# Performance work log

Measured on AMD Instinct MI355X. Metric: run time of the kernel, lower is better.

The kernel has to match this reference:

```python
import jax, jax.numpy as jnp
import numpy as np

D_MODEL = 1024
H = 16
D_K = D_MODEL // H  # 64


def setup_inputs() -> dict:
    key = jax.random.key(0)
    ks = jax.random.split(key, 10)
    s = 1.0 / np.sqrt(D_MODEL)
    x = jax.random.normal(ks[0], (4, 2048, D_MODEL), dtype=jnp.float32)
    # Per-head linear weights stacked: [H, d_model, d_k]
    Wq = jax.random.uniform(ks[1], (H, D_MODEL, D_K), jnp.float32, -s, s)
    bq = jax.random.uniform(ks[2], (H, D_K), jnp.float32, -s, s)
    Wk = jax.random.uniform(ks[3], (H, D_MODEL, D_K), jnp.float32, -s, s)
    bk = jax.random.uniform(ks[4], (H, D_K), jnp.float32, -s, s)
    Wv = jax.random.uniform(ks[5], (H, D_MODEL, D_K), jnp.float32, -s, s)
    bv = jax.random.uniform(ks[6], (H, D_K), jnp.float32, -s, s)
    so = 1.0 / np.sqrt(H * D_K)
    Wo = jax.random.uniform(ks[7], (H * D_K, D_MODEL), jnp.float32, -so, so)
    bo = jax.random.uniform(ks[8], (D_MODEL,), jnp.float32, -so, so)
    return {"x": x, "Wq": Wq, "bq": bq, "Wk": Wk, "bk": bk, "Wv": Wv, "bv": bv, "Wo": Wo, "bo": bo}


def reference(x, Wq, bq, Wk, bk, Wv, bv, Wo, bo):
    # x: [B, S, D]; Wq/Wk/Wv: [H, D, d_k]; b*: [H, d_k]
    q = jnp.einsum('bsd,hdk->bhsk', x, Wq) + bq[None, :, None, :]
    k = jnp.einsum('bsd,hdk->bhsk', x, Wk) + bk[None, :, None, :]
    v = jnp.einsum('bsd,hdk->bhsk', x, Wv) + bv[None, :, None, :]
    scores = jnp.einsum('bhqk,bhsk->bhqs', q, k) / np.sqrt(D_K)
    S = x.shape[1]
    causal = jnp.triu(jnp.ones((S, S), dtype=bool), k=1)  # True above diagonal
    scores = jnp.where(causal, -jnp.inf, scores)
    attn = jax.nn.softmax(scores, axis=-1)
    ctx = jnp.einsum('bhqs,bhsk->bhqk', attn, v)  # [B, H, S, d_k]
    B = x.shape[0]
    # concat heads: torch cats head outputs along last dim -> [B, S, H*d_k]
    ctx = jnp.transpose(ctx, (0, 2, 1, 3)).reshape(B, S, H * D_K)
    return ctx @ Wo + bo
```

## Files before the change

### kernel.cpp

```cpp
#include <hip/hip_runtime.h>
#include <hip/hip_bf16.h>

typedef unsigned short u16;
typedef __attribute__((ext_vector_type(8))) short short8;
typedef __attribute__((ext_vector_type(4))) short short4v;
typedef __attribute__((ext_vector_type(4))) float floatx4;

#define D_MODEL 1024
#define NH 16
#define SEQ 2048
#define BATCH 4
#define M_ROWS 8192
#define N_QKV 3072
#define PS_LD 72

#define QSCALE 0.18033688011112042f
#define EXP2_OFF 11.541560327111707f

__device__ __forceinline__ u16 f2u(float f) {
    __hip_bfloat16 h = __float2bfloat16(f);
    u16 u; __builtin_memcpy(&u, &h, 2); return u;
}

__device__ __forceinline__ void async_copy16(const u16* g, u16* l) {
    __builtin_amdgcn_global_load_lds(
        (const __attribute__((address_space(1))) unsigned int*)(g),
        (__attribute__((address_space(3))) unsigned int*)(l),
        16, 0, 0);
}

__global__ __launch_bounds__(256) void prep(
    const float* __restrict__ x,
    const float* __restrict__ Wq, const float* __restrict__ Wk,
    const float* __restrict__ Wv, const float* __restrict__ Wo,
    const float* __restrict__ bq, const float* __restrict__ bk,
    const float* __restrict__ bv, const float* __restrict__ bo,
    u16* __restrict__ xb, u16* __restrict__ Wpt, u16* __restrict__ Wot,
    float* __restrict__ biasp)
{
    __shared__ u16 T[64 * 72];
    const int tid = threadIdx.x;
    const int blk = blockIdx.x;

    if (blk < 4096) {
        size_t i = ((size_t)blk * 256 + tid) * 8;
        float4 f0 = *(const float4*)&x[i];
        float4 f1 = *(const float4*)&x[i + 4];
        u16 t[8] = {f2u(f0.x), f2u(f0.y), f2u(f0.z), f2u(f0.w),
                    f2u(f1.x), f2u(f1.y), f2u(f1.z), f2u(f1.w)};
        *(short8*)&xb[i] = *(short8*)t;
        return;
    }
    if (blk == 5120) {
        #pragma unroll
        for (int j = 0; j < 16; j++) {
            int idx = j * 256 + tid;
            float v;
            if (idx < 1024)      v = bq[idx] * QSCALE;
            else if (idx < 2048) v = bk[idx - 1024];
            else if (idx < 3072) v = bv[idx - 2048];
            else                 v = bo[idx - 3072];
            biasp[idx] = v;
        }
        return;
    }
    const int wb = blk - 4096;
    const int r = tid >> 2, s4 = (tid & 3) * 16;
    if (wb < 768) {
        int sel = wb / 256, rem = wb % 256;
        int h = rem >> 4, ktile = rem & 15;
        const float* W = (sel == 0) ? Wq : ((sel == 1) ? Wk : Wv);
        const float scale = (sel == 0) ? QSCALE : 1.0f;
        const float* src = W + ((size_t)h * 1024 + ktile * 64 + r) * 64 + s4;
        #pragma unroll
        for (int i = 0; i < 16; i++) T[(s4 + i) * 72 + r] = f2u(src[i] * scale);
        __syncthreads();
        u16 tmp[16];
        #pragma unroll
        for (int i = 0; i < 16; i++) tmp[i] = T[r * 72 + s4 + i];
        u16* dst = Wpt + ((size_t)sel * 1024 + h * 64 + r) * 1024 + ktile * 64 + s4;
        *(short8*)&dst[0] = *(short8*)&tmp[0];
        *(short8*)&dst[8] = *(short8*)&tmp[8];
    } else {
        int rem = wb - 768;
        int nt = rem >> 4, kt2 = rem & 15;
        const float* src = Wo + ((size_t)kt2 * 64 + r) * 1024 + nt * 64 + s4;
        #pragma unroll
        for (int i = 0; i < 16; i++) T[(s4 + i) * 72 + r] = f2u(src[i]);
        __syncthreads();
        u16 tmp[16];
        #pragma unroll
        for (int i = 0; i < 16; i++) tmp[i] = T[r * 72 + s4 + i];
        u16* dst = Wot + ((size_t)nt * 64 + r) * 1024 + kt2 * 64 + s4;
        *(short8*)&dst[0] = *(short8*)&tmp[0];
        *(short8*)&dst[8] = *(short8*)&tmp[8];
    }
}

__global__ __launch_bounds__(256) void vtrans(const u16* __restrict__ QKV,
                                              u16* __restrict__ Vtg) {
    __shared__ u16 T[64 * 72];
    const int bh = blockIdx.x, kt = blockIdx.y;
    const int b = bh >> 4, h = bh & 15;
    const int tid = threadIdx.x;
    const int r = tid >> 2, s4 = (tid & 3) * 16;
    const u16* vp = QKV + (size_t)(b * SEQ + kt * 64 + r) * N_QKV + 2 * D_MODEL + h * 64 + s4;
    *(short8*)&T[r * 72 + s4]     = *(const short8*)&vp[0];
    *(short8*)&T[r * 72 + s4 + 8] = *(const short8*)&vp[8];
    __syncthreads();
    u16 tmp[16];
    #pragma unroll
    for (int i = 0; i < 16; i++) tmp[i] = T[(s4 + i) * 72 + r];
    u16* op = Vtg + ((size_t)bh * 64 + r) * SEQ + kt * 64 + s4;
    *(short8*)&op[0] = *(short8*)&tmp[0];
    *(short8*)&op[8] = *(short8*)&tmp[8];
}

template <typename OT>
__global__ __launch_bounds__(256) void gemm128(
    const u16* __restrict__ A, const u16* __restrict__ Bt,
    const float* __restrict__ bias, OT* __restrict__ C,
    int M, int N, int K)
{
    __shared__ u16 As[128 * 64];
    __shared__ u16 Bs[128 * 64];
    const int tid = threadIdx.x;
    const int w = tid >> 6, lane = tid & 63;
    const int l16 = lane & 15, quad = lane >> 4;

    const int nwgx = gridDim.x;
    const int nwg = nwgx * gridDim.y;
    const int lin = blockIdx.y * nwgx + blockIdx.x;
    const int cpx = nwg >> 3;
    const int swz = (lin & 7) * cpx + (lin >> 3);
    const int bn = (swz % nwgx) * 128, bm = (swz / nwgx) * 128;

    const int wr = (w >> 1) * 64, wc = (w & 1) * 64;

    floatx4 acc[4][4];
    #pragma unroll
    for (int i = 0; i < 4; i++)
        #pragma unroll
        for (int j = 0; j < 4; j++) acc[i][j] = (floatx4){0.f, 0.f, 0.f, 0.f};

    for (int k0 = 0; k0 < K; k0 += 64) {
        #pragma unroll
        for (int c = 0; c < 4; c++) {
            const int off = (w * 4 + c) * 1024 + lane * 16;
            const int row = off >> 7, seg = (off >> 4) & 7;
            async_copy16(A  + (size_t)(bm + row) * K + k0 + seg * 8, &As[(w * 4 + c) * 512]);
            async_copy16(Bt + (size_t)(bn + row) * K + k0 + seg * 8, &Bs[(w * 4 + c) * 512]);
        }
        __syncthreads();
        #pragma unroll
        for (int kc = 0; kc < 2; kc++) {
            short8 a[4], b[4];
            #pragma unroll
            for (int i = 0; i < 4; i++)
                a[i] = *(short8*)&As[(wr + i * 16 + l16) * 64 + kc * 32 + quad * 8];
            #pragma unroll
            for (int i = 0; i < 4; i++)
                b[i] = *(short8*)&Bs[(wc + i * 16 + l16) * 64 + kc * 32 + quad * 8];
            #pragma unroll
            for (int mm = 0; mm < 4; mm++)
                #pragma unroll
                for (int nn = 0; nn < 4; nn++)
                    acc[mm][nn] = __builtin_amdgcn_mfma_f32_16x16x32_bf16(
                        a[mm], b[nn], acc[mm][nn], 0, 0, 0);
        }
        __syncthreads();
    }

    #pragma unroll
    for (int nn = 0; nn < 4; nn++) {
        const int col = bn + wc + nn * 16 + l16;
        const float bi = bias[col];
        #pragma unroll
        for (int mm = 0; mm < 4; mm++) {
            const int row = bm + wr + mm * 16 + quad * 4;
            #pragma unroll
            for (int r = 0; r < 4; r++) {
                float v = acc[mm][nn][r] + bi;
                if constexpr (sizeof(OT) == 2) ((u16*)C)[(size_t)(row + r) * N + col] = f2u(v);
                else                           C[(size_t)(row + r) * N + col] = v;
            }
        }
    }
}

#define G256_BAR   __builtin_amdgcn_s_barrier()
#define G256_LGKM(n) { asm volatile("s_waitcnt lgkmcnt(" #n ")" ::: "memory"); \
                       __builtin_amdgcn_sched_barrier(0); }

#define G256_STG(dstbase, s0, s1) { \
    async_copy16((s0), &lds[(dstbase) + stw]); \
    async_copy16((s1), &lds[(dstbase) + 4096 + stw]); }

#define G256_STAGE_A(bb, half, kq) \
    G256_STG((bb) * 32768 + (half) * 8192, \
             pA[0] + (size_t)(half) * hstep + (kq), \
             pA[1] + (size_t)(half) * hstep + (kq))

#define G256_STAGE_B(bb, half, kq) \
    G256_STG((bb) * 32768 + 16384 + (half) * 8192, \
             pB[0] + (size_t)(half) * hstep + (kq), \
             pB[1] + (size_t)(half) * hstep + (kq))

#define G256_LDA4(dst, bb, mi0) { \
    const int _b = (bb) * 32768 + wm * 8192; \
    _Pragma("unroll") \
    for (int mi = 0; mi < 4; mi++) { \
        const int _r = _b + (((mi0) + mi) * 16 + l16) * 64; \
        dst[mi * 2]     = *(const short8*)&lds[_r + col0]; \
        dst[mi * 2 + 1] = *(const short8*)&lds[_r + col1]; \
    } }

#define G256_LDB2(dst, bb, ni0) { \
    const int _b = (bb) * 32768 + 16384 + (wn >> 1) * 8192 + (wn & 1) * 4096; \
    _Pragma("unroll") \
    for (int ni = 0; ni < 2; ni++) { \
        const int _r = _b + (((ni0) + ni) * 16 + l16) * 64; \
        dst[ni * 2]     = *(const short8*)&lds[_r + col0]; \
        dst[ni * 2 + 1] = *(const short8*)&lds[_r + col1]; \
    } }

#define G256_MMA8(av, bv, MI0, NI0) { \
    _Pragma("unroll") \
    for (int mi = 0; mi < 4; mi++) \
    _Pragma("unroll") \
    for (int ni = 0; ni < 2; ni++) { \
        acc[(MI0) + mi][(NI0) + ni] = __builtin_amdgcn_mfma_f32_16x16x32_bf16( \
            bv[ni * 2],     av[mi * 2],     acc[(MI0) + mi][(NI0) + ni], 0, 0, 0); \
        acc[(MI0) + mi][(NI0) + ni] = __builtin_amdgcn_mfma_f32_16x16x32_bf16( \
            bv[ni * 2 + 1], av[mi * 2 + 1], acc[(MI0) + mi][(NI0) + ni], 0, 0, 0); \
    } }

template <typename OT>
__global__ __launch_bounds__(512, 2) void gemm256(
    const u16* __restrict__ A, const u16* __restrict__ Bt,
    const float* __restrict__ bias, OT* __restrict__ C,
    int M, int N, int K)
{
    __shared__ u16 lds[65536];
    const int tid = threadIdx.x;
    const int w = tid >> 6, lane = tid & 63;
    const int l16 = lane & 15, quad = lane >> 4;
    const int wm = w >> 2, wn = w & 3;

    const int nwgx = gridDim.x;
    const int nwg = nwgx * gridDim.y;
    const int lin = blockIdx.y * nwgx + blockIdx.x;
    const int cpx = nwg >> 3;
    const int swz = (lin & 7) * cpx + (lin >> 3);
    const int bn = (swz % nwgx) * 256, bm = (swz / nwgx) * 256;

    const u16* pA[2]; const u16* pB[2];
    #pragma unroll
    for (int j = 0; j < 2; j++) {
        const int d = (j * 512 + tid) * 16;
        const int s = d ^ (((d >> 7) & 7) << 4);
        const int r = s >> 7;
        const int c = (s & 127) >> 1;
        pA[j] = A  + (size_t)(bm + r) * K + c;
        pB[j] = Bt + (size_t)(bn + r) * K + c;
    }
    const size_t hstep = (size_t)128 * K;
    const int stw = w * 512;

    const int xm = (l16 & 7) << 3;
    const int col0 = (quad * 8) ^ xm;
    const int col1 = (32 + quad * 8) ^ xm;

    floatx4 acc[8][4];
    #pragma unroll
    for (int i = 0; i < 8; i++)
        #pragma unroll
        for (int j = 0; j < 4; j++) acc[i][j] = (floatx4){0.f, 0.f, 0.f, 0.f};

    G256_STAGE_A(0, 0, 0);  G256_STAGE_A(0, 1, 0);
    G256_STAGE_B(0, 0, 0);  G256_STAGE_B(0, 1, 0);
    G256_STAGE_B(1, 0, 64); G256_STAGE_B(1, 1, 64);
    G256_STAGE_A(1, 0, 64);
    asm volatile("s_waitcnt vmcnt(6)" ::: "memory");
    __syncthreads();

    short8 a0[8], a1[8], b0[4], b1[4];
    G256_LDA4(a0, 0, 0);
    G256_LDB2(b0, 0, 0);

    const int NKT = K >> 6;
    for (int kt = 0; kt < NKT; ++kt) {
        const int buf = kt & 1, nb = buf ^ 1;
        const int kqA = (kt + 1) << 6, kqB = (kt + 2) << 6;
        const bool st1 = (kt + 1 < NKT), st2 = (kt + 2 < NKT);

        G256_LDB2(b1, buf, 2);
        if (st1) { G256_STAGE_A(nb, 1, kqA); }
        G256_BAR; G256_LGKM(4);
        __builtin_amdgcn_s_setprio(1); G256_MMA8(a0, b0, 0, 0);
        __builtin_amdgcn_s_setprio(0); G256_BAR;

        G256_LDA4(a1, buf, 4);
        G256_BAR; G256_LGKM(8);
        __builtin_amdgcn_s_setprio(1); G256_MMA8(a0, b1, 0, 2);
        __builtin_amdgcn_s_setprio(0); G256_BAR;

        if (st2) { G256_STAGE_B(buf, 0, kqB); }
        G256_BAR; G256_LGKM(0);
        __builtin_amdgcn_s_setprio(1); G256_MMA8(a1, b0, 4, 0);
        __builtin_amdgcn_s_setprio(0); G256_BAR;

        if (st2) { G256_STAGE_B(buf, 1, kqB); G256_STAGE_A(buf, 0, kqB); }
        if (st1) {
            if (st2) { asm volatile("s_waitcnt vmcnt(6)" ::: "memory"); }
            else     { asm volatile("s_waitcnt vmcnt(0)" ::: "memory"); }
            __builtin_amdgcn_sched_barrier(0);
            G256_LDA4(a0, nb, 0);
            G256_LDB2(b0, nb, 0);
        }
        G256_BAR;
        __builtin_amdgcn_s_setprio(1); G256_MMA8(a1, b1, 4, 2);
        __builtin_amdgcn_s_setprio(0); G256_BAR;
    }

    float4 bi[4];
    #pragma unroll
    for (int ni = 0; ni < 4; ni++)
        bi[ni] = *(const float4*)&bias[bn + wn * 64 + ni * 16 + quad * 4];
    #pragma unroll
    for (int mi = 0; mi < 8; mi++) {
        const int row = bm + wm * 128 + mi * 16 + l16;
        #pragma unroll
        for (int ni = 0; ni < 4; ni++) {
            const int col = bn + wn * 64 + ni * 16 + quad * 4;
            const float v0 = acc[mi][ni][0] + bi[ni].x;
            const float v1 = acc[mi][ni][1] + bi[ni].y;
            const float v2 = acc[mi][ni][2] + bi[ni].z;
            const float v3 = acc[mi][ni][3] + bi[ni].w;
            if constexpr (sizeof(OT) == 2) {
                u16 o[4] = {f2u(v0), f2u(v1), f2u(v2), f2u(v3)};
                *(short4v*)&((u16*)C)[(size_t)row * N + col] = *(short4v*)o;
            } else {
                float4 fv = {v0, v1, v2, v3};
                *(float4*)&C[(size_t)row * N + col] = fv;
            }
        }
    }
}

__global__ __launch_bounds__(256) void attn_mfma(
    const u16* __restrict__ QKV, const u16* __restrict__ Vtg, u16* __restrict__ ctx)
{
    __shared__ u16 Ks[2][64 * 64];
    __shared__ u16 Vs[2][64 * 64];
    __shared__ u16 Ps[128 * PS_LD];

    const int bh = blockIdx.x;
    const int qt = (int)(gridDim.y - 1) - (int)blockIdx.y;
    const int b = bh >> 4, h = bh & 15;
    const int tid = threadIdx.x;
    const int w = tid >> 6, lane = tid & 63;
    const int l16 = lane & 15, quad = lane >> 4;

    const int r0 = tid >> 3,        c0 = tid & 7;
    const int r1 = (256 + tid) >> 3, c1 = tid & 7;
    const int sw0 = c0 ^ (r0 & 7), sw1 = c1 ^ (r1 & 7);

    short8 q[2][2];
    #pragma unroll
    for (int m = 0; m < 2; m++) {
        const u16* qp = QKV + (size_t)(b * SEQ + qt * 128 + w * 32 + m * 16 + l16) * N_QKV + h * 64;
        q[m][0] = *(const short8*)&qp[quad * 8];
        q[m][1] = *(const short8*)&qp[32 + quad * 8];
    }

    short8 ones8;
    #pragma unroll
    for (int i = 0; i < 8; i++) ones8[i] = (short)0x3F80;

    floatx4 O[2][4];
    floatx4 lsum[2];
    #pragma unroll
    for (int m = 0; m < 2; m++) {
        lsum[m] = (floatx4){0.f, 0.f, 0.f, 0.f};
        #pragma unroll
        for (int i = 0; i < 4; i++) O[m][i] = (floatx4){0.f, 0.f, 0.f, 0.f};
    }

    const int nkt = 2 * qt + 2;
    const int qrow_w_max = qt * 128 + w * 32 + 31;

    const size_t kbase = (size_t)(b * SEQ) * N_QKV + D_MODEL + h * 64;
    const size_t vbase = (size_t)bh * 64 * SEQ;

    const u16* kpa = QKV + kbase + (size_t)r0 * N_QKV + c0 * 8;
    const u16* kpb = QKV + kbase + (size_t)r1 * N_QKV + c1 * 8;
    const u16* vpa = Vtg + vbase + (size_t)r0 * SEQ + c0 * 8;
    const u16* vpb = Vtg + vbase + (size_t)r1 * SEQ + c1 * 8;

    {
        float4 ka = *(const float4*)kpa;
        float4 kb = *(const float4*)kpb;
        float4 va = *(const float4*)vpa;
        float4 vb = *(const float4*)vpb;
        *(float4*)&Ks[0][r0 * 64 + sw0 * 8] = ka;
        *(float4*)&Ks[0][r1 * 64 + sw1 * 8] = kb;
        *(float4*)&Vs[0][r0 * 64 + sw0 * 8] = va;
        *(float4*)&Vs[0][r1 * 64 + sw1 * 8] = vb;
    }
    kpa += (size_t)64 * N_QKV; kpb += (size_t)64 * N_QKV;
    vpa += 64; vpb += 64;
    __syncthreads();

    for (int kt = 0; kt < nkt; kt++) {
        const int buf = kt & 1;
        const bool pre = (kt + 1 < nkt);
        float4 ka, kb, va, vb;
        if (pre) {
            ka = *(const float4*)kpa;
            kb = *(const float4*)kpb;
            va = *(const float4*)vpa;
            vb = *(const float4*)vpb;
            kpa += (size_t)64 * N_QKV; kpb += (size_t)64 * N_QKV;
            vpa += 64; vpb += 64;
        }

        if (kt * 64 <= qrow_w_max) {
            short8 kf[4][2];
            #pragma unroll
            for (int ns = 0; ns < 4; ns++) {
                const int rr = ns * 16 + l16, rs = rr & 7;
                kf[ns][0] = *(short8*)&Ks[buf][rr * 64 + (quad ^ rs) * 8];
                kf[ns][1] = *(short8*)&Ks[buf][rr * 64 + ((4 + quad) ^ rs) * 8];
            }
            const bool needMask = (kt * 64 + 63 > qt * 128 + w * 32);

            #pragma unroll
            for (int m = 0; m < 2; m++) {
                floatx4 z[4];
                __builtin_amdgcn_s_setprio(1);
                #pragma unroll
                for (int ns = 0; ns < 4; ns++) {
                    floatx4 t = (floatx4){0.f, 0.f, 0.f, 0.f};
                    t = __builtin_amdgcn_mfma_f32_16x16x32_bf16(kf[ns][0], q[m][0], t, 0, 0, 0);
                    t = __builtin_amdgcn_mfma_f32_16x16x32_bf16(kf[ns][1], q[m][1], t, 0, 0, 0);
                    z[ns] = t;
                }
                __builtin_amdgcn_s_setprio(0);
                const int qrow_g = qt * 128 + w * 32 + m * 16 + l16;
                const int prow = (w * 32 + m * 16 + l16) * PS_LD;
                #pragma unroll
                for (int ns = 0; ns < 4; ns++) {
                    u16 pk[4];
                    #pragma unroll
                    for (int r = 0; r < 4; r++) {
                        float s = z[ns][r];
                        const int key = kt * 64 + ns * 16 + quad * 4 + r;
                        if (needMask && key > qrow_g) s = -INFINITY;
                        float p = __builtin_amdgcn_exp2f(s - EXP2_OFF);
                        pk[r] = f2u(p);
                    }
                    *(short4v*)&Ps[prow + ns * 16 + quad * 4] = *(short4v*)pk;
                }
            }

            short8 vf[4][2];
            #pragma unroll
            for (int ds = 0; ds < 4; ds++) {
                const int rr = ds * 16 + l16, rs = rr & 7;
                vf[ds][0] = *(short8*)&Vs[buf][rr * 64 + (quad ^ rs) * 8];
                vf[ds][1] = *(short8*)&Vs[buf][rr * 64 + ((4 + quad) ^ rs) * 8];
            }
            __builtin_amdgcn_s_setprio(1);
            #pragma unroll
            for (int m = 0; m < 2; m++) {
                const int prow = (w * 32 + m * 16 + l16) * PS_LD;
                short8 p0 = *(short8*)&Ps[prow + quad * 8];
                short8 p1 = *(short8*)&Ps[prow + 32 + quad * 8];
                lsum[m] = __builtin_amdgcn_mfma_f32_16x16x32_bf16(ones8, p0, lsum[m], 0, 0, 0);
                lsum[m] = __builtin_amdgcn_mfma_f32_16x16x32_bf16(ones8, p1, lsum[m], 0, 0, 0);
                #pragma unroll
                for (int ds = 0; ds < 4; ds++) {
                    O[m][ds] = __builtin_amdgcn_mfma_f32_16x16x32_bf16(vf[ds][0], p0, O[m][ds], 0, 0, 0);
                    O[m][ds] = __builtin_amdgcn_mfma_f32_16x16x32_bf16(vf[ds][1], p1, O[m][ds], 0, 0, 0);
                }
            }
            __builtin_amdgcn_s_setprio(0);
        }

        if (pre) {
            const int nb = buf ^ 1;
            *(float4*)&Ks[nb][r0 * 64 + sw0 * 8] = ka;
            *(float4*)&Ks[nb][r1 * 64 + sw1 * 8] = kb;
            *(float4*)&Vs[nb][r0 * 64 + sw0 * 8] = va;
            *(float4*)&Vs[nb][r1 * 64 + sw1 * 8] = vb;
        }
        __syncthreads();
    }

    #pragma unroll
    for (int m = 0; m < 2; m++) {
        const float inv = 1.0f / lsum[m][0];
        const size_t base = (size_t)(b * SEQ + qt * 128 + w * 32 + m * 16 + l16) * D_MODEL + h * 64;
        #pragma unroll
        for (int ds = 0; ds < 4; ds++) {
            u16 o[4];
            #pragma unroll
            for (int r = 0; r < 4; r++) o[r] = f2u(O[m][ds][r] * inv);
            *(short4v*)&ctx[base + ds * 16 + quad * 4] = *(short4v*)o;
        }
    }
}

extern "C" void kernel_launch(void* const* d_in, const int* in_sizes, int n_in,
                              void* d_out, int out_size, void* d_ws, size_t ws_size,
                              hipStream_t stream) {
    const float* x  = (const float*)d_in[0];
    const float* Wq = (const float*)d_in[1];
    const float* bq = (const float*)d_in[2];
    const float* Wk = (const float*)d_in[3];
    const float* bk = (const float*)d_in[4];
    const float* Wv = (const float*)d_in[5];
    const float* bv = (const float*)d_in[6];
    const float* Wo = (const float*)d_in[7];
    const float* bo = (const float*)d_in[8];
    float* out = (float*)d_out;

    char* ws = (char*)d_ws;
    float* biasp = (float*)ws;
    u16*   Wpt   = (u16*)(ws + 0x10000);
    u16*   Wot   = (u16*)(ws + 0x620000);
    u16*   xb    = (u16*)(ws + 0x840000);
    u16*   Vtg   = xb;
    u16*   QKV   = (u16*)(ws + 0x1840000);
    u16*   ctx   = (u16*)(ws + 0x4840000);

    prep<<<5121, 256, 0, stream>>>(x, Wq, Wk, Wv, Wo, bq, bk, bv, bo,
                                   xb, Wpt, Wot, biasp);

    gemm256<u16><<<dim3(N_QKV / 256, M_ROWS / 256), 512, 0, stream>>>(
        xb, Wpt, biasp, QKV, M_ROWS, N_QKV, D_MODEL);

    vtrans<<<dim3(64, 32), 256, 0, stream>>>(QKV, Vtg);

    attn_mfma<<<dim3(BATCH * NH, SEQ / 128), 256, 0, stream>>>(QKV, Vtg, ctx);

    gemm128<float><<<dim3(D_MODEL / 128, M_ROWS / 128), 256, 0, stream>>>(
        ctx, Wot, biasp + N_QKV, out, M_ROWS, D_MODEL, D_MODEL);
}
```

Before: 284.1 us.

## Retile QKV GEMM to 256x192 blocks to balance waves across CUs

The QKV projection GEMM moves from 256x256 tiles to 256x192 tiles, so the grid goes from 12x32=384 to 16x32=512 workgroups. The staging, LDS layout and MFMA schedule are reworked for three 64-row B chunks: each warp now computes 8x3 accumulator tiles, with a new single-column B load and a four-MFMA step. The aim is better balance across the 256 CUs (two full waves instead of a partial one) and a smaller LDS footprint. The cost is lower arithmetic intensity per tile and a less symmetric pipeline, with different vmcnt wait counts.

After: 273.7 us. -3.7%, faster.

```diff
diff --git a/kernel.cpp b/kernel.cpp
--- a/kernel.cpp
+++ b/kernel.cpp
@@ -192,22 +192,16 @@
 #define G256_LGKM(n) { asm volatile("s_waitcnt lgkmcnt(" #n ")" ::: "memory"); \
                        __builtin_amdgcn_sched_barrier(0); }
 
-#define G256_STG(dstbase, s0, s1) { \
-    async_copy16((s0), &lds[(dstbase) + stw]); \
-    async_copy16((s1), &lds[(dstbase) + 4096 + stw]); }
-
-#define G256_STAGE_A(bb, half, kq) \
-    G256_STG((bb) * 32768 + (half) * 8192, \
-             pA[0] + (size_t)(half) * hstep + (kq), \
-             pA[1] + (size_t)(half) * hstep + (kq))
-
-#define G256_STAGE_B(bb, half, kq) \
-    G256_STG((bb) * 32768 + 16384 + (half) * 8192, \
-             pB[0] + (size_t)(half) * hstep + (kq), \
-             pB[1] + (size_t)(half) * hstep + (kq))
-
-#define G256_LDA4(dst, bb, mi0) { \
-    const int _b = (bb) * 32768 + wm * 8192; \
+#define GQ_STAGE_A(bb, ca, kq) \
+    async_copy16(pAc + (size_t)(ca) * 64 * K + (kq), \
+                 &lds[(bb) * 28672 + (ca) * 4096 + stw]);
+
+#define GQ_STAGE_B(bb, cb, kq) \
+    async_copy16(pBc + (size_t)(cb) * 64 * K + (kq), \
+                 &lds[(bb) * 28672 + 16384 + (cb) * 4096 + stw]);
+
+#define GQ_LDA4(dst, bb, mi0) { \
+    const int _b = (bb) * 28672 + wm * 8192; \
     _Pragma("unroll") \
     for (int mi = 0; mi < 4; mi++) { \
         const int _r = _b + (((mi0) + mi) * 16 + l16) * 64; \
@@ -215,8 +209,8 @@
         dst[mi * 2 + 1] = *(const short8*)&lds[_r + col1]; \
     } }
 
-#define G256_LDB2(dst, bb, ni0) { \
-    const int _b = (bb) * 32768 + 16384 + (wn >> 1) * 8192 + (wn & 1) * 4096; \
+#define GQ_LDB2(dst, bb, ni0) { \
+    const int _b = (bb) * 28672 + 16384 + wn * 3072; \
     _Pragma("unroll") \
     for (int ni = 0; ni < 2; ni++) { \
         const int _r = _b + (((ni0) + ni) * 16 + l16) * 64; \
@@ -224,7 +218,13 @@
         dst[ni * 2 + 1] = *(const short8*)&lds[_r + col1]; \
     } }
 
-#define G256_MMA8(av, bv, MI0, NI0) { \
+#define GQ_LDB1(dst, bb, ni0) { \
+    const int _b = (bb) * 28672 + 16384 + wn * 3072; \
+    const int _r = _b + ((ni0) * 16 + l16) * 64; \
+    dst[0] = *(const short8*)&lds[_r + col0]; \
+    dst[1] = *(const short8*)&lds[_r + col1]; }
+
+#define GQ_MMA8(av, bv, MI0, NI0) { \
     _Pragma("unroll") \
     for (int mi = 0; mi < 4; mi++) \
     _Pragma("unroll") \
@@ -235,13 +235,22 @@
             bv[ni * 2 + 1], av[mi * 2 + 1], acc[(MI0) + mi][(NI0) + ni], 0, 0, 0); \
     } }
 
+#define GQ_MMA4(av, bv, MI0) { \
+    _Pragma("unroll") \
+    for (int mi = 0; mi < 4; mi++) { \
+        acc[(MI0) + mi][2] = __builtin_amdgcn_mfma_f32_16x16x32_bf16( \
+            bv[0], av[mi * 2],     acc[(MI0) + mi][2], 0, 0, 0); \
+        acc[(MI0) + mi][2] = __builtin_amdgcn_mfma_f32_16x16x32_bf16( \
+            bv[1], av[mi * 2 + 1], acc[(MI0) + mi][2], 0, 0, 0); \
+    } }
+
 template <typename OT>
-__global__ __launch_bounds__(512, 2) void gemm256(
+__global__ __launch_bounds__(512, 2) void gemm_qkv(
     const u16* __restrict__ A, const u16* __restrict__ Bt,
     const float* __restrict__ bias, OT* __restrict__ C,
     int M, int N, int K)
 {
-    __shared__ u16 lds[65536];
+    __shared__ u16 lds[57344];
     const int tid = threadIdx.x;
     const int w = tid >> 6, lane = tid & 63;
     const int l16 = lane & 15, quad = lane >> 4;
@@ -252,41 +261,35 @@
     const int lin = blockIdx.y * nwgx + blockIdx.x;
     const int cpx = nwg >> 3;
     const int swz = (lin & 7) * cpx + (lin >> 3);
-    const int bn = (swz % nwgx) * 256, bm = (swz / nwgx) * 256;
-
-    const u16* pA[2]; const u16* pB[2];
-    #pragma unroll
-    for (int j = 0; j < 2; j++) {
-        const int d = (j * 512 + tid) * 16;
-        const int s = d ^ (((d >> 7) & 7) << 4);
-        const int r = s >> 7;
-        const int c = (s & 127) >> 1;
-        pA[j] = A  + (size_t)(bm + r) * K + c;
-        pB[j] = Bt + (size_t)(bn + r) * K + c;
-    }
-    const size_t hstep = (size_t)128 * K;
+    const int bn = (swz % nwgx) * 192, bm = (swz / nwgx) * 256;
+
+    const int d = tid * 16;
+    const int s = d ^ (((d >> 7) & 7) << 4);
+    const int r = s >> 7;
+    const int c = (s & 127) >> 1;
+    const u16* pAc = A  + (size_t)(bm + r) * K + c;
+    const u16* pBc = Bt + (size_t)(bn + r) * K + c;
     const int stw = w * 512;
 
     const int xm = (l16 & 7) << 3;
     const int col0 = (quad * 8) ^ xm;
     const int col1 = (32 + quad * 8) ^ xm;
 
-    floatx4 acc[8][4];
+    floatx4 acc[8][3];
     #pragma unroll
     for (int i = 0; i < 8; i++)
         #pragma unroll
-        for (int j = 0; j < 4; j++) acc[i][j] = (floatx4){0.f, 0.f, 0.f, 0.f};
-
-    G256_STAGE_A(0, 0, 0);  G256_STAGE_A(0, 1, 0);
-    G256_STAGE_B(0, 0, 0);  G256_STAGE_B(0, 1, 0);
-    G256_STAGE_B(1, 0, 64); G256_STAGE_B(1, 1, 64);
-    G256_STAGE_A(1, 0, 64);
-    asm volatile("s_waitcnt vmcnt(6)" ::: "memory");
+        for (int j = 0; j < 3; j++) acc[i][j] = (floatx4){0.f, 0.f, 0.f, 0.f};
+
+    GQ_STAGE_A(0, 0, 0); GQ_STAGE_A(0, 1, 0); GQ_STAGE_A(0, 2, 0); GQ_STAGE_A(0, 3, 0);
+    GQ_STAGE_B(0, 0, 0); GQ_STAGE_B(0, 1, 0); GQ_STAGE_B(0, 2, 0);
+    GQ_STAGE_B(1, 0, 64); GQ_STAGE_B(1, 1, 64); GQ_STAGE_B(1, 2, 64);
+    asm volatile("s_waitcnt vmcnt(3)" ::: "memory");
     __syncthreads();
 
-    short8 a0[8], a1[8], b0[4], b1[4];
-    G256_LDA4(a0, 0, 0);
-    G256_LDB2(b0, 0, 0);
+    short8 a0[8], a1[8], b0[4], b1[2];
+    GQ_LDA4(a0, 0, 0);
+    GQ_LDB2(b0, 0, 0);
 
     const int NKT = K >> 6;
     for (int kt = 0; kt < NKT; ++kt) {
@@ -294,45 +297,46 @@
         const int kqA = (kt + 1) << 6, kqB = (kt + 2) << 6;
         const bool st1 = (kt + 1 < NKT), st2 = (kt + 2 < NKT);
 
-        G256_LDB2(b1, buf, 2);
-        if (st1) { G256_STAGE_A(nb, 1, kqA); }
-        G256_BAR; G256_LGKM(4);
-        __builtin_amdgcn_s_setprio(1); G256_MMA8(a0, b0, 0, 0);
+        GQ_LDB1(b1, buf, 2);
+        if (st1) { GQ_STAGE_A(nb, 0, kqA); GQ_STAGE_A(nb, 1, kqA); }
+        G256_BAR; G256_LGKM(2);
+        __builtin_amdgcn_s_setprio(1); GQ_MMA8(a0, b0, 0, 0);
         __builtin_amdgcn_s_setprio(0); G256_BAR;
 
-        G256_LDA4(a1, buf, 4);
+        GQ_LDA4(a1, buf, 4);
+        if (st1) { GQ_STAGE_A(nb, 2, kqA); GQ_STAGE_A(nb, 3, kqA); }
         G256_BAR; G256_LGKM(8);
-        __builtin_amdgcn_s_setprio(1); G256_MMA8(a0, b1, 0, 2);
+        __builtin_amdgcn_s_setprio(1); GQ_MMA4(a0, b1, 0);
         __builtin_amdgcn_s_setprio(0); G256_BAR;
 
-        if (st2) { G256_STAGE_B(buf, 0, kqB); }
+        if (st2) { GQ_STAGE_B(buf, 0, kqB); GQ_STAGE_B(buf, 1, kqB); }
         G256_BAR; G256_LGKM(0);
-        __builtin_amdgcn_s_setprio(1); G256_MMA8(a1, b0, 4, 0);
+        __builtin_amdgcn_s_setprio(1); GQ_MMA8(a1, b0, 4, 0);
         __builtin_amdgcn_s_setprio(0); G256_BAR;
 
-        if (st2) { G256_STAGE_B(buf, 1, kqB); G256_STAGE_A(buf, 0, kqB); }
+        if (st2) { GQ_STAGE_B(buf, 2, kqB); }
         if (st1) {
-            if (st2) { asm volatile("s_waitcnt vmcnt(6)" ::: "memory"); }
+            if (st2) { asm volatile("s_waitcnt vmcnt(3)" ::: "memory"); }
             else     { asm volatile("s_waitcnt vmcnt(0)" ::: "memory"); }
             __builtin_amdgcn_sched_barrier(0);
-            G256_LDA4(a0, nb, 0);
-            G256_LDB2(b0, nb, 0);
+            GQ_LDA4(a0, nb, 0);
+            GQ_LDB2(b0, nb, 0);
         }
         G256_BAR;
-        __builtin_amdgcn_s_setprio(1); G256_MMA8(a1, b1, 4, 2);
+        __builtin_amdgcn_s_setprio(1); GQ_MMA4(a1, b1, 4);
         __builtin_amdgcn_s_setprio(0); G256_BAR;
     }
 
-    float4 bi[4];
-    #pragma unroll
-    for (int ni = 0; ni < 4; ni++)
-        bi[ni] = *(const float4*)&bias[bn + wn * 64 + ni * 16 + quad * 4];
+    float4 bi[3];
+    #pragma unroll
+    for (int ni = 0; ni < 3; ni++)
+        bi[ni] = *(const float4*)&bias[bn + wn * 48 + ni * 16 + quad * 4];
     #pragma unroll
     for (int mi = 0; mi < 8; mi++) {
         const int row = bm + wm * 128 + mi * 16 + l16;
         #pragma unroll
-        for (int ni = 0; ni < 4; ni++) {
-            const int col = bn + wn * 64 + ni * 16 + quad * 4;
+        for (int ni = 0; ni < 3; ni++) {
+            const int col = bn + wn * 48 + ni * 16 + quad * 4;
             const float v0 = acc[mi][ni][0] + bi[ni].x;
             const float v1 = acc[mi][ni][1] + bi[ni].y;
             const float v2 = acc[mi][ni][2] + bi[ni].z;
@@ -538,7 +542,7 @@
     prep<<<5121, 256, 0, stream>>>(x, Wq, Wk, Wv, Wo, bq, bk, bv, bo,
                                    xb, Wpt, Wot, biasp);
 
-    gemm256<u16><<<dim3(N_QKV / 256, M_ROWS / 256), 512, 0, stream>>>(
+    gemm_qkv<u16><<<dim3(N_QKV / 192, M_ROWS / 256), 512, 0, stream>>>(
         xb, Wpt, biasp, QKV, M_ROWS, N_QKV, D_MODEL);
 
     vtrans<<<dim3(64, 32), 256, 0, stream>>>(QKV, Vtg);
```
